# Kernel tuning notes

Hardware: AMD Instinct MI355X
Metric: run time of the kernel (lower is better)

The kernel has to match this reference:

```python
import jax, jax.numpy as jnp
import numpy as np

B, D, H = 512, 1024, 2048          # batch, context_dim, l_hidden
MAX_STEPS = 8                       # config.max_l_steps
ATOL = 0.01                         # config.l_conv_atol
THR = 0.1                           # config.commitment_threshold


def setup_inputs() -> dict:
    key = jax.random.key(0)
    ks = jax.random.split(key, 20)
    mat = lambda k, shp, fi: jax.random.normal(k, shp, jnp.float32) / np.float32(np.sqrt(fi))
    inp = dict(
        enc=jax.random.normal(ks[0], (B, D), jnp.float32),
        static_context=jax.random.normal(ks[1], (B, D), jnp.float32),
        # fresh RWKV state: channel 3 (pp, running max-exponent) = -1e30
        l_state=jnp.zeros((B, H, 5), jnp.float32).at[:, :, 3].set(-1e30),
        initial_drift=0.1 * jax.random.normal(ks[2], (B, D), jnp.float32),
        # l_input_proj: Linear(2*D -> H)
        Win=mat(ks[3], (2 * D, H), 2 * D), b_in=jnp.zeros((H,), jnp.float32),
        # context_drift_proj: Linear(H -> D, bias=False)
        Wdrift=mat(ks[4], (H, D), H),
        # l_to_out: Linear(H -> D)
        Wout=mat(ks[5], (H, D), H), b_out=jnp.zeros((D,), jnp.float32),
        # RWKV cell (v4-style) parameters over hidden dim H
        mix_k=jax.random.uniform(ks[6], (H,), jnp.float32),
        mix_v=jax.random.uniform(ks[7], (H,), jnp.float32),
        mix_r=jax.random.uniform(ks[8], (H,), jnp.float32),
        mix_k2=jax.random.uniform(ks[9], (H,), jnp.float32),
        mix_r2=jax.random.uniform(ks[10], (H,), jnp.float32),
        time_decay=0.5 * jax.random.normal(ks[11], (H,), jnp.float32),
        time_first=0.5 * jax.random.normal(ks[12], (H,), jnp.float32),
        Wk=mat(ks[13], (H, H), H), Wv=mat(ks[14], (H, H), H),
        Wr=mat(ks[15], (H, H), H), Wo=mat(ks[16], (H, H), H),
        Wk2=mat(ks[17], (H, H), H), Wv2=mat(ks[18], (H, H), H),
        Wr2=mat(ks[19], (H, H), H),
    )
    return inp


def _forward(enc, static_context, l_state, initial_drift, Win, b_in, Wdrift, Wout, b_out,
             mix_k, mix_v, mix_r, mix_k2, mix_r2, time_decay, time_first,
             Wk, Wv, Wr, Wo, Wk2, Wv2, Wr2):
    def cell(x, state):
        # RWKV-style linear-attention cell. state: [B,H,5] = (x_prev_tm, aa, bb, pp, x_prev_cm)
        xx, aa, bb, pp, cc = (state[..., i] for i in range(5))
        xk = x * mix_k + xx * (1.0 - mix_k)
        xv = x * mix_v + xx * (1.0 - mix_v)
        xr = x * mix_r + xx * (1.0 - mix_r)
        r = jax.nn.sigmoid(xr @ Wr)
        k = xk @ Wk
        v = xv @ Wv
        ww = time_first + k
        q = jnp.maximum(pp, ww)
        e1 = jnp.exp(pp - q); e2 = jnp.exp(ww - q)
        wkv = (e1 * aa + e2 * v) / (e1 * bb + e2)
        ww2 = pp - jnp.exp(time_decay)
        q2 = jnp.maximum(ww2, k)
        e1b = jnp.exp(ww2 - q2); e2b = jnp.exp(k - q2)
        tm_out = (r * wkv) @ Wo
        # channel-mix half of the cell (state channel 4)
        xk2 = x * mix_k2 + cc * (1.0 - mix_k2)
        xr2 = x * mix_r2 + cc * (1.0 - mix_r2)
        r2 = jax.nn.sigmoid(xr2 @ Wr2)
        kk = jnp.square(jax.nn.relu(xk2 @ Wk2))
        out = tm_out + r2 * (kk @ Wv2)
        new_state = jnp.stack([x, e1b * aa + e2b * v, e1b * bb + e2b, q2, x], axis=-1)
        return out, new_state

    def l_input_of(drift):
        v = jnp.concatenate([enc, static_context + drift], axis=-1) @ Win + b_in
        return jnp.clip(v, -50.0, 50.0)

    def step(carry, _):
        drift, sstate, done, csum, cnt = carry
        li = l_input_of(drift)
        out, ns = cell(li, sstate)
        ns = jnp.clip(ns, -50.0, 50.0)
        delta = jnp.tanh(out @ Wdrift)
        nd = jnp.clip(drift + delta, -5.0, 5.0)
        hinge = jnp.minimum(jax.nn.relu(jnp.mean(jnp.sum(nd * nd, axis=-1)) - THR), 100.0)
        conv = jnp.mean(jnp.abs(delta)) < ATOL
        # freeze all updates once converged (early-exit semantics under jit)
        drift = jnp.where(done, drift, nd)
        sstate = jnp.where(done, sstate, ns)
        csum = jnp.where(done, csum, csum + hinge)
        cnt = jnp.where(done, cnt, cnt + 1.0)
        done = jnp.logical_or(done, conv)
        return (drift, sstate, done, csum, cnt), None

    carry0 = (initial_drift, l_state, jnp.array(False), jnp.float32(0.0), jnp.float32(0.0))
    (drift, _, _, csum, cnt), _ = jax.lax.scan(step, carry0, None, length=MAX_STEPS)

    # final commit step uses the ORIGINAL l_state (not the shadow state)
    li = l_input_of(drift)
    final_out, next_state = cell(li, l_state)
    next_state = jnp.clip(next_state, -50.0, 50.0)
    final_enc = enc + final_out @ Wout + b_out
    commitment = csum / jnp.maximum(cnt, 1.0)
    return final_enc, next_state, commitment, drift


def reference(enc, static_context, l_state, initial_drift, Win, b_in, Wdrift, Wout, b_out,
              mix_k, mix_v, mix_r, mix_k2, mix_r2, time_decay, time_first,
              Wk, Wv, Wr, Wo, Wk2, Wv2, Wr2):
    return _forward(enc, static_context, l_state, initial_drift, Win, b_in, Wdrift, Wout, b_out,
                    mix_k, mix_v, mix_r, mix_k2, mix_r2, time_decay, time_first,
                    Wk, Wv, Wr, Wo, Wk2, Wv2, Wr2)
```

## Files before the change

kernel.cpp:

```cpp
#include <hip/hip_runtime.h>
#include <hip/hip_bf16.h>

#define Bb 512
#define Dd 1024
#define Hh 2048
#define BH_ (Bb*Hh)
#define BD_ (Bb*Dd)

typedef unsigned short u16;
typedef __attribute__((ext_vector_type(8))) short short8;
typedef __attribute__((ext_vector_type(4))) float f32x4;

enum { M_F32 = 0, M_IN, M_SIG, M_SQRELU, M_OUT, M_DRIFT, M_FINAL };

struct GemmP {
    const u16* A[3];
    const u16* W[3];
    void* dst[3];
    int mode[3];
    int M, N, K;
    const int* done;
    const float* bias;
    const float* mk; const float* mv; const float* mr; const float* mk2v; const float* mr2v;
    const float* xx; const float* cc;
    const float* lstate;
    float* liF;
    float* stateOut;
    u16 *o1, *o2, *o3, *o4, *o5;
    const float* f1; const float* f2;
    float* drift; float* accAbs; float* accSq;
    float* scal; int nticket;
    const float* enc; const float* bout; float* dout;
};

__global__ __launch_bounds__(512, 4) void gemm_sk(GemmP p) {
    if (p.done && *(volatile const int*)p.done) return;
    const int z = blockIdx.z;
    const u16* __restrict__ A = p.A[z];
    const u16* __restrict__ W = p.W[z];
    const int Kd = p.K;
    const int m0 = blockIdx.y * 64, n0 = blockIdx.x * 64;

    __shared__ alignas(16) u16 As[64 * 136];
    __shared__ alignas(16) u16 Bs[64 * 136];

    const int t = threadIdx.x;
    const int l = t & 63, w = t >> 6;
    const int lane16 = l & 15, quad = l >> 4;
    const int wq = w & 3, kg = w >> 2;
    const int wm = wq & 1, wn = wq >> 1;
    const int srow = t >> 3, scp = t & 7;

    f32x4 zero = {0.f, 0.f, 0.f, 0.f};
    f32x4 acc[2][2];
    acc[0][0] = zero; acc[0][1] = zero; acc[1][0] = zero; acc[1][1] = zero;

    const u16* ap = A + (size_t)(m0 + srow) * Kd + scp * 8;
    const u16* bp = W + (size_t)(n0 + srow) * Kd + scp * 8;

    uint4 ra0 = *(const uint4*)(const void*)(ap);
    uint4 ra1 = *(const uint4*)(const void*)(ap + 64);
    uint4 rb0 = *(const uint4*)(const void*)(bp);
    uint4 rb1 = *(const uint4*)(const void*)(bp + 64);

    for (int k0 = 0; k0 < Kd; k0 += 128) {
        *(uint4*)(void*)&As[srow * 136 + scp * 8]      = ra0;
        *(uint4*)(void*)&As[srow * 136 + scp * 8 + 64] = ra1;
        *(uint4*)(void*)&Bs[srow * 136 + scp * 8]      = rb0;
        *(uint4*)(void*)&Bs[srow * 136 + scp * 8 + 64] = rb1;
        __syncthreads();
        if (k0 + 128 < Kd) {
            ra0 = *(const uint4*)(const void*)(ap + k0 + 128);
            ra1 = *(const uint4*)(const void*)(ap + k0 + 192);
            rb0 = *(const uint4*)(const void*)(bp + k0 + 128);
            rb1 = *(const uint4*)(const void*)(bp + k0 + 192);
        }
        const int kb = kg * 64;
#pragma unroll
        for (int kc = 0; kc < 64; kc += 32) {
            const int col = kb + kc + quad * 8;
            short8 af0 = *(const short8*)(const void*)&As[(wm * 32 + lane16) * 136 + col];
            short8 af1 = *(const short8*)(const void*)&As[(wm * 32 + 16 + lane16) * 136 + col];
            short8 bf0 = *(const short8*)(const void*)&Bs[(wn * 32 + lane16) * 136 + col];
            short8 bf1 = *(const short8*)(const void*)&Bs[(wn * 32 + 16 + lane16) * 136 + col];
            acc[0][0] = __builtin_amdgcn_mfma_f32_16x16x32_bf16(af0, bf0, acc[0][0], 0, 0, 0);
            acc[0][1] = __builtin_amdgcn_mfma_f32_16x16x32_bf16(af0, bf1, acc[0][1], 0, 0, 0);
            acc[1][0] = __builtin_amdgcn_mfma_f32_16x16x32_bf16(af1, bf0, acc[1][0], 0, 0, 0);
            acc[1][1] = __builtin_amdgcn_mfma_f32_16x16x32_bf16(af1, bf1, acc[1][1], 0, 0, 0);
        }
        __syncthreads();
    }

    float* red = (float*)As;
    const int rbase = wq * 1088 + l * 17;
    if (kg == 1) {
#pragma unroll
        for (int sm = 0; sm < 2; ++sm)
#pragma unroll
            for (int sn = 0; sn < 2; ++sn)
#pragma unroll
                for (int i = 0; i < 4; ++i)
                    red[rbase + (sm * 2 + sn) * 4 + i] = acc[sm][sn][i];
    }
    __syncthreads();
    if (kg == 0) {
#pragma unroll
        for (int sm = 0; sm < 2; ++sm)
#pragma unroll
            for (int sn = 0; sn < 2; ++sn)
#pragma unroll
                for (int i = 0; i < 4; ++i)
                    acc[sm][sn][i] += red[rbase + (sm * 2 + sn) * 4 + i];
    }

    const int mode = p.mode[z];
    float sabs = 0.f, ssq = 0.f;
    if (kg == 0) {
#pragma unroll
        for (int sm = 0; sm < 2; ++sm)
#pragma unroll
            for (int sn = 0; sn < 2; ++sn)
#pragma unroll
                for (int i = 0; i < 4; ++i) {
                    const int m = m0 + wm * 32 + sm * 16 + quad * 4 + i;
                    const int n = n0 + wn * 32 + sn * 16 + lane16;
                    const size_t idx = (size_t)m * p.N + n;
                    const float v = acc[sm][sn][i];
                    if (mode == M_F32) {
                        ((float*)p.dst[z])[idx] = v;
                    } else if (mode == M_IN) {
                        float li = fminf(fmaxf(v + p.bias[n], -50.f), 50.f);
                        float xxv, ccv;
                        if (p.lstate) { xxv = p.lstate[idx * 5 + 0]; ccv = p.lstate[idx * 5 + 4]; }
                        else { xxv = p.xx[idx]; ccv = p.cc[idx]; }
                        float mk = p.mk[n], mv = p.mv[n], mr = p.mr[n], mk2 = p.mk2v[n], mr2 = p.mr2v[n];
                        ((__hip_bfloat16*)p.o1)[idx] = __float2bfloat16(li * mk + xxv * (1.f - mk));
                        ((__hip_bfloat16*)p.o2)[idx] = __float2bfloat16(li * mv + xxv * (1.f - mv));
                        ((__hip_bfloat16*)p.o3)[idx] = __float2bfloat16(li * mr + xxv * (1.f - mr));
                        ((__hip_bfloat16*)p.o4)[idx] = __float2bfloat16(li * mk2 + ccv * (1.f - mk2));
                        ((__hip_bfloat16*)p.o5)[idx] = __float2bfloat16(li * mr2 + ccv * (1.f - mr2));
                        if (p.lstate) { p.stateOut[idx * 5 + 0] = li; p.stateOut[idx * 5 + 4] = li; }
                        else p.liF[idx] = li;
                    } else if (mode == M_SIG) {
                        ((float*)p.dst[z])[idx] = 1.f / (1.f + __expf(-v));
                    } else if (mode == M_SQRELU) {
                        float r = fmaxf(v, 0.f);
                        ((__hip_bfloat16*)p.dst[z])[idx] = __float2bfloat16(r * r);
                    } else if (mode == M_OUT) {
                        ((__hip_bfloat16*)p.dst[z])[idx] = __float2bfloat16(p.f1[idx] + p.f2[idx] * v);
                    } else if (mode == M_DRIFT) {
                        float d = tanhf(v);
                        float nd = fminf(fmaxf(p.drift[idx] + d, -5.f), 5.f);
                        p.drift[idx] = nd;
                        sabs += fabsf(d);
                        ssq += nd * nd;
                    } else {
                        p.dout[idx] = p.enc[idx] + v + p.bout[n];
                    }
                }
    }
    if (mode == M_DRIFT) {
        if (kg == 0) {
#pragma unroll
            for (int off = 32; off > 0; off >>= 1) {
                sabs += __shfl_down(sabs, off, 64);
                ssq += __shfl_down(ssq, off, 64);
            }
            if (l == 0) { atomicAdd(p.accAbs, sabs); atomicAdd(p.accSq, ssq); }
        }
        __syncthreads();
        if (t == 0) {
            __threadfence();
            int v = atomicAdd((int*)(p.scal + 5), 1);
            if (v == p.nticket - 1) {
                volatile float* s = p.scal;
                float hinge = fminf(fmaxf(s[4] / (float)Bb - 0.1f, 0.f), 100.f);
                s[1] = s[1] + hinge;
                s[2] = s[2] + 1.f;
                if (s[3] / (float)BD_ < 0.01f) ((volatile int*)p.scal)[0] = 1;
                s[3] = 0.f; s[4] = 0.f;
                ((volatile int*)p.scal)[5] = 0;
            }
        }
    }
}

__global__ void transposeW(const float* __restrict__ src, u16* __restrict__ dst, int K, int N) {
    __shared__ float tile[32][33];
    int kt = blockIdx.y * 32, nt = blockIdx.x * 32;
    int tx = threadIdx.x, ty = threadIdx.y;
#pragma unroll
    for (int j = 0; j < 4; j++)
        tile[ty + j * 8][tx] = src[(size_t)(kt + ty + j * 8) * N + nt + tx];
    __syncthreads();
    __hip_bfloat16* d = (__hip_bfloat16*)dst;
#pragma unroll
    for (int j = 0; j < 4; j++)
        d[(size_t)(nt + ty + j * 8) * K + kt + tx] = __float2bfloat16(tile[tx][ty + j * 8]);
}

__global__ void initstate(const float* __restrict__ lstate, const float* __restrict__ idrift,
                          float* xx, float* aa, float* bb, float* pp, float* cc,
                          float* drift, float* scal) {
    int i = blockIdx.x * 256 + threadIdx.x;
    if (i < BH_) {
        const float* s = lstate + (size_t)i * 5;
        xx[i] = s[0]; aa[i] = s[1]; bb[i] = s[2]; pp[i] = s[3]; cc[i] = s[4];
    }
    if (i < BD_) drift[i] = idrift[i];
    if (i == 0) {
        ((int*)scal)[0] = 0; scal[1] = 0.f; scal[2] = 0.f; scal[3] = 0.f; scal[4] = 0.f;
        ((int*)scal)[5] = 0;
    }
}

__global__ void prep(const float* __restrict__ enc, const float* __restrict__ sc,
                     const float* __restrict__ drift, u16* __restrict__ Acat, const int* done) {
    if (done && *(volatile const int*)done) return;
    int i = blockIdx.x * 256 + threadIdx.x;
    if (i >= BD_) return;
    int m = i >> 10, d = i & 1023;
    __hip_bfloat16* Ab = (__hip_bfloat16*)Acat;
    Ab[(size_t)m * 2048 + d] = __float2bfloat16(enc[i]);
    Ab[(size_t)m * 2048 + 1024 + d] = __float2bfloat16(sc[i] + drift[i]);
}

__global__ void mix1(const float* __restrict__ Kp, const float* __restrict__ Vp,
                     const float* __restrict__ Rp,
                     float* aa, float* bb, float* pp, float* xx, float* cc,
                     const float* __restrict__ Li,
                     const float* __restrict__ tf, const float* __restrict__ td,
                     u16* __restrict__ rwkv,
                     const float* __restrict__ lstate, float* stateOut,
                     const int* done) {
    if (done && *(volatile const int*)done) return;
    int i = blockIdx.x * 256 + threadIdx.x;
    if (i >= BH_) return;
    int h = i & (Hh - 1);
    float k = Kp[i], v = Vp[i], rpre = Rp[i];
    float a, b, P;
    if (lstate) { a = lstate[(size_t)i * 5 + 1]; b = lstate[(size_t)i * 5 + 2]; P = lstate[(size_t)i * 5 + 3]; }
    else { a = aa[i]; b = bb[i]; P = pp[i]; }
    float r = 1.f / (1.f + __expf(-rpre));
    float ww = tf[h] + k;
    float q = fmaxf(P, ww);
    float e1 = __expf(P - q), e2 = __expf(ww - q);
    float wkv = (e1 * a + e2 * v) / (e1 * b + e2);
    ((__hip_bfloat16*)rwkv)[i] = __float2bfloat16(r * wkv);
    float ww2 = P - __expf(td[h]);
    float q2 = fmaxf(ww2, k);
    float e1b = __expf(ww2 - q2), e2b = __expf(k - q2);
    float na = fminf(fmaxf(e1b * a + e2b * v, -50.f), 50.f);
    float nb = fminf(fmaxf(e1b * b + e2b, -50.f), 50.f);
    float nq = fminf(fmaxf(q2, -50.f), 50.f);
    if (lstate) {
        stateOut[(size_t)i * 5 + 1] = na; stateOut[(size_t)i * 5 + 2] = nb; stateOut[(size_t)i * 5 + 3] = nq;
    } else {
        aa[i] = na; bb[i] = nb; pp[i] = nq;
        float li = Li[i];
        xx[i] = li; cc[i] = li;
    }
}

__global__ void tailk(const float* __restrict__ scal, const float* __restrict__ drift, float* __restrict__ dout) {
    int i = blockIdx.x * 256 + threadIdx.x;
    const size_t OC = (size_t)BD_ + (size_t)5 * BH_;
    if (i == 0) dout[OC] = scal[1] / fmaxf(scal[2], 1.f);
    if (i < BD_) dout[OC + 1 + i] = drift[i];
}

extern "C" void kernel_launch(void* const* d_in, const int* in_sizes, int n_in,
                              void* d_out, int out_size, void* d_ws, size_t ws_size,
                              hipStream_t stream) {
    const float* enc    = (const float*)d_in[0];
    const float* sc     = (const float*)d_in[1];
    const float* lstate = (const float*)d_in[2];
    const float* idrift = (const float*)d_in[3];
    const float* Win    = (const float*)d_in[4];
    const float* b_in   = (const float*)d_in[5];
    const float* Wdrift = (const float*)d_in[6];
    const float* Wout   = (const float*)d_in[7];
    const float* b_out  = (const float*)d_in[8];
    const float* mix_k  = (const float*)d_in[9];
    const float* mix_v  = (const float*)d_in[10];
    const float* mix_r  = (const float*)d_in[11];
    const float* mix_k2 = (const float*)d_in[12];
    const float* mix_r2 = (const float*)d_in[13];
    const float* tdec   = (const float*)d_in[14];
    const float* tfirst = (const float*)d_in[15];
    const float* Wk  = (const float*)d_in[16];
    const float* Wv  = (const float*)d_in[17];
    const float* Wr  = (const float*)d_in[18];
    const float* Wo  = (const float*)d_in[19];
    const float* Wk2 = (const float*)d_in[20];
    const float* Wv2 = (const float*)d_in[21];
    const float* Wr2 = (const float*)d_in[22];
    float* dout = (float*)d_out;

    const size_t BHs = (size_t)Bb * Hh;
    const size_t BDs = (size_t)Bb * Dd;

    const size_t need_f32 = 9 * BHs + BDs + 16;
    const size_t need_u16 = (size_t)2 * Dd * Hh + 7 * (size_t)Hh * Hh + 2 * (size_t)Hh * Dd + 8 * BHs;
    const size_t need_bytes = need_f32 * 4 + need_u16 * 2;
    if (ws_size < need_bytes) return;

    float* f = (float*)d_ws;
    float* xx  = f;
    float* aa  = xx + BHs;
    float* bbp = aa + BHs;
    float* ppp = bbp + BHs;
    float* cc  = ppp + BHs;
    float* Li  = cc + BHs;
    float* Kp  = Li + BHs;
    float* Vp  = Kp + BHs;
    float* Rp  = Vp + BHs;
    float* Tm  = Kp;
    float* R2  = Vp;
    float* drift = Rp + BHs;
    float* scal  = drift + BDs;
    u16* u = (u16*)(scal + 16);
    u16* WinT  = u; u += (size_t)2 * Dd * Hh;
    u16* WkT   = u; u += (size_t)Hh * Hh;
    u16* WvT   = u; u += (size_t)Hh * Hh;
    u16* WrT   = u; u += (size_t)Hh * Hh;
    u16* WoT   = u; u += (size_t)Hh * Hh;
    u16* Wk2T  = u; u += (size_t)Hh * Hh;
    u16* Wv2T  = u; u += (size_t)Hh * Hh;
    u16* Wr2T  = u; u += (size_t)Hh * Hh;
    u16* WdT   = u; u += (size_t)Hh * Dd;
    u16* WoutT = u; u += (size_t)Hh * Dd;
    u16* Acat = u; u += BHs;
    u16* Xk   = u; u += BHs;
    u16* Xv   = u; u += BHs;
    u16* Xr   = u; u += BHs;
    u16* Xk2  = u; u += BHs;
    u16* Xr2  = u; u += BHs;
    u16* Rw   = u; u += BHs;
    u16* Kk   = u; u += BHs;
    u16* Ob   = Acat;

    int* doneptr = (int*)scal;
    float* accAbs = scal + 3;
    float* accSq  = scal + 4;

    dim3 tb(32, 8);
    transposeW<<<dim3(Hh / 32, (2 * Dd) / 32), tb, 0, stream>>>(Win, WinT, 2 * Dd, Hh);
    transposeW<<<dim3(Hh / 32, Hh / 32), tb, 0, stream>>>(Wk,  WkT,  Hh, Hh);
    transposeW<<<dim3(Hh / 32, Hh / 32), tb, 0, stream>>>(Wv,  WvT,  Hh, Hh);
    transposeW<<<dim3(Hh / 32, Hh / 32), tb, 0, stream>>>(Wr,  WrT,  Hh, Hh);
    transposeW<<<dim3(Hh / 32, Hh / 32), tb, 0, stream>>>(Wo,  WoT,  Hh, Hh);
    transposeW<<<dim3(Hh / 32, Hh / 32), tb, 0, stream>>>(Wk2, Wk2T, Hh, Hh);
    transposeW<<<dim3(Hh / 32, Hh / 32), tb, 0, stream>>>(Wv2, Wv2T, Hh, Hh);
    transposeW<<<dim3(Hh / 32, Hh / 32), tb, 0, stream>>>(Wr2, Wr2T, Hh, Hh);
    transposeW<<<dim3(Dd / 32, Hh / 32), tb, 0, stream>>>(Wdrift, WdT, Hh, Dd);
    transposeW<<<dim3(Dd / 32, Hh / 32), tb, 0, stream>>>(Wout, WoutT, Hh, Dd);

    initstate<<<(BH_ + 255) / 256, 256, 0, stream>>>(lstate, idrift, xx, aa, bbp, ppp, cc, drift, scal);

    GemmP p1 = {};
    p1.A[0] = Acat; p1.W[0] = WinT; p1.mode[0] = M_IN;
    p1.M = Bb; p1.N = Hh; p1.K = 2 * Dd;
    p1.done = doneptr;
    p1.bias = b_in; p1.mk = mix_k; p1.mv = mix_v; p1.mr = mix_r; p1.mk2v = mix_k2; p1.mr2v = mix_r2;
    p1.xx = xx; p1.cc = cc; p1.liF = Li;
    p1.o1 = Xk; p1.o2 = Xv; p1.o3 = Xr; p1.o4 = Xk2; p1.o5 = Xr2;

    GemmP p2 = {};
    p2.A[0] = Xk; p2.A[1] = Xv; p2.A[2] = Xr;
    p2.W[0] = WkT; p2.W[1] = WvT; p2.W[2] = WrT;
    p2.mode[0] = M_F32; p2.mode[1] = M_F32; p2.mode[2] = M_F32;
    p2.dst[0] = Kp; p2.dst[1] = Vp; p2.dst[2] = Rp;
    p2.M = Bb; p2.N = Hh; p2.K = Hh;
    p2.done = doneptr;

    GemmP p3 = {};
    p3.A[0] = Rw; p3.A[1] = Xr2; p3.A[2] = Xk2;
    p3.W[0] = WoT; p3.W[1] = Wr2T; p3.W[2] = Wk2T;
    p3.mode[0] = M_F32; p3.mode[1] = M_SIG; p3.mode[2] = M_SQRELU;
    p3.dst[0] = Tm; p3.dst[1] = R2; p3.dst[2] = Kk;
    p3.M = Bb; p3.N = Hh; p3.K = Hh;
    p3.done = doneptr;

    GemmP p4 = {};
    p4.A[0] = Kk; p4.W[0] = Wv2T; p4.mode[0] = M_OUT; p4.dst[0] = Ob;
    p4.M = Bb; p4.N = Hh; p4.K = Hh;
    p4.f1 = Tm; p4.f2 = R2;
    p4.done = doneptr;

    GemmP p5 = {};
    p5.A[0] = Ob; p5.W[0] = WdT; p5.mode[0] = M_DRIFT;
    p5.M = Bb; p5.N = Dd; p5.K = Hh;
    p5.drift = drift; p5.accAbs = accAbs; p5.accSq = accSq;
    p5.scal = scal; p5.nticket = (Dd / 64) * (Bb / 64);
    p5.done = doneptr;

    dim3 gH(Hh / 64, Bb / 64, 1);
    dim3 gH3(Hh / 64, Bb / 64, 3);
    dim3 gD(Dd / 64, Bb / 64, 1);

    for (int s = 0; s < 8; ++s) {
        prep<<<(BD_ + 255) / 256, 256, 0, stream>>>(enc, sc, drift, Acat, doneptr);
        gemm_sk<<<gH, 512, 0, stream>>>(p1);
        gemm_sk<<<gH3, 512, 0, stream>>>(p2);
        mix1<<<(BH_ + 255) / 256, 256, 0, stream>>>(Kp, Vp, Rp, aa, bbp, ppp, xx, cc, Li,
                                                    tfirst, tdec, Rw, nullptr, nullptr, doneptr);
        gemm_sk<<<gH3, 512, 0, stream>>>(p3);
        gemm_sk<<<gH, 512, 0, stream>>>(p4);
        gemm_sk<<<gD, 512, 0, stream>>>(p5);
    }

    float* stateOut = dout + BD_;

    prep<<<(BD_ + 255) / 256, 256, 0, stream>>>(enc, sc, drift, Acat, nullptr);

    GemmP f1p = p1;
    f1p.done = nullptr; f1p.lstate = lstate; f1p.stateOut = stateOut;
    gemm_sk<<<gH, 512, 0, stream>>>(f1p);

    GemmP f2p = p2; f2p.done = nullptr;
    gemm_sk<<<gH3, 512, 0, stream>>>(f2p);

    mix1<<<(BH_ + 255) / 256, 256, 0, stream>>>(Kp, Vp, Rp, aa, bbp, ppp, xx, cc, Li,
                                                tfirst, tdec, Rw, lstate, stateOut, nullptr);

    GemmP f3p = p3; f3p.done = nullptr;
    gemm_sk<<<gH3, 512, 0, stream>>>(f3p);

    GemmP f4p = p4; f4p.done = nullptr;
    gemm_sk<<<gH, 512, 0, stream>>>(f4p);

    GemmP f5p = {};
    f5p.A[0] = Ob; f5p.W[0] = WoutT; f5p.mode[0] = M_FINAL;
    f5p.M = Bb; f5p.N = Dd; f5p.K = Hh;
    f5p.enc = enc; f5p.bout = b_out; f5p.dout = dout;
    gemm_sk<<<gD, 512, 0, stream>>>(f5p);

    tailk<<<(BD_ + 255) / 256, 256, 0, stream>>>(scal, drift, dout);
}
```

Before: 1.686 ms.

## Shrink GEMM M-tile to 32 with 4-way split-K and batch weight transposes

The GEMM block tile drops from 64x64 to 32x64 rows while the K step per stage grows to 256, split across four K-groups of two warps each. A three-way shared-memory reduction merges the partial sums. The grids double in the M dimension to raise block count and occupancy for these small-batch GEMMs, and the launch bound is raised to 6 blocks per CU. The ten separate weight-transpose launches are merged into one batched launch that skips out-of-range tiles, though each tile of A is now reused across fewer columns.

Result: slower. 1.768 ms (+4.9%).

```diff
diff --git a/kernel.cpp b/kernel.cpp
--- a/kernel.cpp
+++ b/kernel.cpp
@@ -33,56 +33,62 @@
     const float* enc; const float* bout; float* dout;
 };
 
-__global__ __launch_bounds__(512, 4) void gemm_sk(GemmP p) {
+__global__ __launch_bounds__(512, 6) void gemm_sk(GemmP p) {
     if (p.done && *(volatile const int*)p.done) return;
     const int z = blockIdx.z;
     const u16* __restrict__ A = p.A[z];
     const u16* __restrict__ W = p.W[z];
     const int Kd = p.K;
-    const int m0 = blockIdx.y * 64, n0 = blockIdx.x * 64;
-
-    __shared__ alignas(16) u16 As[64 * 136];
-    __shared__ alignas(16) u16 Bs[64 * 136];
+    const int m0 = blockIdx.y * 32, n0 = blockIdx.x * 64;
+
+    __shared__ alignas(16) u16 S[(32 + 64) * 264];
+    u16* As = S;
+    u16* Bs = S + 32 * 264;
 
     const int t = threadIdx.x;
     const int l = t & 63, w = t >> 6;
     const int lane16 = l & 15, quad = l >> 4;
-    const int wq = w & 3, kg = w >> 2;
-    const int wm = wq & 1, wn = wq >> 1;
-    const int srow = t >> 3, scp = t & 7;
+    const int wn = w & 1, kg = w >> 1;
 
     f32x4 zero = {0.f, 0.f, 0.f, 0.f};
     f32x4 acc[2][2];
     acc[0][0] = zero; acc[0][1] = zero; acc[1][0] = zero; acc[1][1] = zero;
 
-    const u16* ap = A + (size_t)(m0 + srow) * Kd + scp * 8;
-    const u16* bp = W + (size_t)(n0 + srow) * Kd + scp * 8;
+    const u16* ap = A + (size_t)(m0 + (t >> 4)) * Kd + (t & 15) * 8;
+    const u16* bp = W + (size_t)(n0 + (t >> 3)) * Kd + (t & 7) * 8;
+    const int aoff = (t >> 4) * 264 + (t & 15) * 8;
+    const int boff = (t >> 3) * 264 + (t & 7) * 8;
 
     uint4 ra0 = *(const uint4*)(const void*)(ap);
-    uint4 ra1 = *(const uint4*)(const void*)(ap + 64);
+    uint4 ra1 = *(const uint4*)(const void*)(ap + 128);
     uint4 rb0 = *(const uint4*)(const void*)(bp);
     uint4 rb1 = *(const uint4*)(const void*)(bp + 64);
-
-    for (int k0 = 0; k0 < Kd; k0 += 128) {
-        *(uint4*)(void*)&As[srow * 136 + scp * 8]      = ra0;
-        *(uint4*)(void*)&As[srow * 136 + scp * 8 + 64] = ra1;
-        *(uint4*)(void*)&Bs[srow * 136 + scp * 8]      = rb0;
-        *(uint4*)(void*)&Bs[srow * 136 + scp * 8 + 64] = rb1;
+    uint4 rb2 = *(const uint4*)(const void*)(bp + 128);
+    uint4 rb3 = *(const uint4*)(const void*)(bp + 192);
+
+    for (int k0 = 0; k0 < Kd; k0 += 256) {
+        *(uint4*)(void*)&As[aoff]       = ra0;
+        *(uint4*)(void*)&As[aoff + 128] = ra1;
+        *(uint4*)(void*)&Bs[boff]       = rb0;
+        *(uint4*)(void*)&Bs[boff + 64]  = rb1;
+        *(uint4*)(void*)&Bs[boff + 128] = rb2;
+        *(uint4*)(void*)&Bs[boff + 192] = rb3;
         __syncthreads();
-        if (k0 + 128 < Kd) {
-            ra0 = *(const uint4*)(const void*)(ap + k0 + 128);
-            ra1 = *(const uint4*)(const void*)(ap + k0 + 192);
-            rb0 = *(const uint4*)(const void*)(bp + k0 + 128);
-            rb1 = *(const uint4*)(const void*)(bp + k0 + 192);
+        if (k0 + 256 < Kd) {
+            ra0 = *(const uint4*)(const void*)(ap + k0 + 256);
+            ra1 = *(const uint4*)(const void*)(ap + k0 + 384);
+            rb0 = *(const uint4*)(const void*)(bp + k0 + 256);
+            rb1 = *(const uint4*)(const void*)(bp + k0 + 320);
+            rb2 = *(const uint4*)(const void*)(bp + k0 + 384);
+            rb3 = *(const uint4*)(const void*)(bp + k0 + 448);
         }
-        const int kb = kg * 64;
 #pragma unroll
         for (int kc = 0; kc < 64; kc += 32) {
-            const int col = kb + kc + quad * 8;
-            short8 af0 = *(const short8*)(const void*)&As[(wm * 32 + lane16) * 136 + col];
-            short8 af1 = *(const short8*)(const void*)&As[(wm * 32 + 16 + lane16) * 136 + col];
-            short8 bf0 = *(const short8*)(const void*)&Bs[(wn * 32 + lane16) * 136 + col];
-            short8 bf1 = *(const short8*)(const void*)&Bs[(wn * 32 + 16 + lane16) * 136 + col];
+            const int col = kg * 64 + kc + quad * 8;
+            short8 af0 = *(const short8*)(const void*)&As[lane16 * 264 + col];
+            short8 af1 = *(const short8*)(const void*)&As[(lane16 + 16) * 264 + col];
+            short8 bf0 = *(const short8*)(const void*)&Bs[(wn * 32 + lane16) * 264 + col];
+            short8 bf1 = *(const short8*)(const void*)&Bs[(wn * 32 + 16 + lane16) * 264 + col];
             acc[0][0] = __builtin_amdgcn_mfma_f32_16x16x32_bf16(af0, bf0, acc[0][0], 0, 0, 0);
             acc[0][1] = __builtin_amdgcn_mfma_f32_16x16x32_bf16(af0, bf1, acc[0][1], 0, 0, 0);
             acc[1][0] = __builtin_amdgcn_mfma_f32_16x16x32_bf16(af1, bf0, acc[1][0], 0, 0, 0);
@@ -91,9 +97,9 @@
         __syncthreads();
     }
 
-    float* red = (float*)As;
-    const int rbase = wq * 1088 + l * 17;
-    if (kg == 1) {
+    float* red = (float*)S;
+    if (kg != 0) {
+        const int rbase = ((kg - 1) * 2 + wn) * 1088 + l * 17;
 #pragma unroll
         for (int sm = 0; sm < 2; ++sm)
 #pragma unroll
@@ -105,12 +111,16 @@
     __syncthreads();
     if (kg == 0) {
 #pragma unroll
-        for (int sm = 0; sm < 2; ++sm)
-#pragma unroll
-            for (int sn = 0; sn < 2; ++sn)
-#pragma unroll
-                for (int i = 0; i < 4; ++i)
-                    acc[sm][sn][i] += red[rbase + (sm * 2 + sn) * 4 + i];
+        for (int s = 0; s < 3; ++s) {
+            const int rbase = (s * 2 + wn) * 1088 + l * 17;
+#pragma unroll
+            for (int sm = 0; sm < 2; ++sm)
+#pragma unroll
+                for (int sn = 0; sn < 2; ++sn)
+#pragma unroll
+                    for (int i = 0; i < 4; ++i)
+                        acc[sm][sn][i] += red[rbase + (sm * 2 + sn) * 4 + i];
+        }
     }
 
     const int mode = p.mode[z];
@@ -122,7 +132,7 @@
             for (int sn = 0; sn < 2; ++sn)
 #pragma unroll
                 for (int i = 0; i < 4; ++i) {
-                    const int m = m0 + wm * 32 + sm * 16 + quad * 4 + i;
+                    const int m = m0 + sm * 16 + quad * 4 + i;
                     const int n = n0 + wn * 32 + sn * 16 + lane16;
                     const size_t idx = (size_t)m * p.N + n;
                     const float v = acc[sm][sn][i];
@@ -185,18 +195,24 @@
     }
 }
 
-__global__ void transposeW(const float* __restrict__ src, u16* __restrict__ dst, int K, int N) {
+struct TransP { const float* s[10]; u16* d[10]; int N[10]; };
+__global__ void transposeAll(TransP tp) {
+    const int z = blockIdx.z;
+    const int N = tp.N[z];
+    const int nt = blockIdx.x * 32;
+    if (nt >= N) return;
+    const int kt = blockIdx.y * 32;
+    const float* __restrict__ src = tp.s[z];
+    __hip_bfloat16* d = (__hip_bfloat16*)tp.d[z];
     __shared__ float tile[32][33];
-    int kt = blockIdx.y * 32, nt = blockIdx.x * 32;
     int tx = threadIdx.x, ty = threadIdx.y;
 #pragma unroll
     for (int j = 0; j < 4; j++)
         tile[ty + j * 8][tx] = src[(size_t)(kt + ty + j * 8) * N + nt + tx];
     __syncthreads();
-    __hip_bfloat16* d = (__hip_bfloat16*)dst;
 #pragma unroll
     for (int j = 0; j < 4; j++)
-        d[(size_t)(nt + ty + j * 8) * K + kt + tx] = __float2bfloat16(tile[tx][ty + j * 8]);
+        d[(size_t)(nt + ty + j * 8) * 2048 + kt + tx] = __float2bfloat16(tile[tx][ty + j * 8]);
 }
 
 __global__ void initstate(const float* __restrict__ lstate, const float* __restrict__ idrift,
@@ -344,17 +360,18 @@
     float* accAbs = scal + 3;
     float* accSq  = scal + 4;
 
-    dim3 tb(32, 8);
-    transposeW<<<dim3(Hh / 32, (2 * Dd) / 32), tb, 0, stream>>>(Win, WinT, 2 * Dd, Hh);
-    transposeW<<<dim3(Hh / 32, Hh / 32), tb, 0, stream>>>(Wk,  WkT,  Hh, Hh);
-    transposeW<<<dim3(Hh / 32, Hh / 32), tb, 0, stream>>>(Wv,  WvT,  Hh, Hh);
-    transposeW<<<dim3(Hh / 32, Hh / 32), tb, 0, stream>>>(Wr,  WrT,  Hh, Hh);
-    transposeW<<<dim3(Hh / 32, Hh / 32), tb, 0, stream>>>(Wo,  WoT,  Hh, Hh);
-    transposeW<<<dim3(Hh / 32, Hh / 32), tb, 0, stream>>>(Wk2, Wk2T, Hh, Hh);
-    transposeW<<<dim3(Hh / 32, Hh / 32), tb, 0, stream>>>(Wv2, Wv2T, Hh, Hh);
-    transposeW<<<dim3(Hh / 32, Hh / 32), tb, 0, stream>>>(Wr2, Wr2T, Hh, Hh);
-    transposeW<<<dim3(Dd / 32, Hh / 32), tb, 0, stream>>>(Wdrift, WdT, Hh, Dd);
-    transposeW<<<dim3(Dd / 32, Hh / 32), tb, 0, stream>>>(Wout, WoutT, Hh, Dd);
+    TransP tp;
+    tp.s[0] = Win;   tp.d[0] = WinT;  tp.N[0] = Hh;
+    tp.s[1] = Wk;    tp.d[1] = WkT;   tp.N[1] = Hh;
+    tp.s[2] = Wv;    tp.d[2] = WvT;   tp.N[2] = Hh;
+    tp.s[3] = Wr;    tp.d[3] = WrT;   tp.N[3] = Hh;
+    tp.s[4] = Wo;    tp.d[4] = WoT;   tp.N[4] = Hh;
+    tp.s[5] = Wk2;   tp.d[5] = Wk2T;  tp.N[5] = Hh;
+    tp.s[6] = Wv2;   tp.d[6] = Wv2T;  tp.N[6] = Hh;
+    tp.s[7] = Wr2;   tp.d[7] = Wr2T;  tp.N[7] = Hh;
+    tp.s[8] = Wdrift; tp.d[8] = WdT;  tp.N[8] = Dd;
+    tp.s[9] = Wout;  tp.d[9] = WoutT; tp.N[9] = Dd;
+    transposeAll<<<dim3(Hh / 32, Hh / 32, 10), dim3(32, 8), 0, stream>>>(tp);
 
     initstate<<<(BH_ + 255) / 256, 256, 0, stream>>>(lstate, idrift, xx, aa, bbp, ppp, cc, drift, scal);
 
@@ -392,12 +409,12 @@
     p5.A[0] = Ob; p5.W[0] = WdT; p5.mode[0] = M_DRIFT;
     p5.M = Bb; p5.N = Dd; p5.K = Hh;
     p5.drift = drift; p5.accAbs = accAbs; p5.accSq = accSq;
-    p5.scal = scal; p5.nticket = (Dd / 64) * (Bb / 64);
+    p5.scal = scal; p5.nticket = (Dd / 64) * (Bb / 32);
     p5.done = doneptr;
 
-    dim3 gH(Hh / 64, Bb / 64, 1);
-    dim3 gH3(Hh / 64, Bb / 64, 3);
-    dim3 gD(Dd / 64, Bb / 64, 1);
+    dim3 gH(Hh / 64, Bb / 32, 1);
+    dim3 gH3(Hh / 64, Bb / 32, 3);
+    dim3 gD(Dd / 64, Bb / 32, 1);
 
     for (int s = 0; s < 8; ++s) {
         prep<<<(BD_ + 255) / 256, 256, 0, stream>>>(enc, sc, drift, Acat, doneptr);
```
